# Kernel optimization log

Measured on AMD Instinct MI355X. Metric: run time of the kernel, lower is better.

## Reference

```python
import jax, jax.numpy as jnp
import numpy as np

S, N, NSUB, F, HID, NH = 8, 20000, 4000, 128, 64, 8


def setup_inputs() -> dict:
    key = jax.random.key(0)
    ks = jax.random.split(key, 24)
    # unique sorted node indices per snapshot (matches snap.nodes used for gather + scatter-pad)
    nodes = jnp.stack([jnp.sort(jax.random.permutation(ks[i], N)[:NSUB]) for i in range(S)])
    # dense normalized adjacency proxy (norm_adj.to_dense()); scaled so rows sum ~1
    adj = jax.random.uniform(ks[8], (S, NSUB, NSUB), dtype=jnp.float32) * (2.0 / NSUB)
    p = lambda k, shp: jax.random.normal(k, shp, dtype=jnp.float32) * 0.02
    return {
        "nodes": nodes,
        "adj": adj,
        "emb": p(ks[9], (N, F)),
        "W1": p(ks[10], (F, HID)), "b1": jnp.zeros((HID,), jnp.float32),
        "W2": p(ks[11], (HID, HID)), "b2": jnp.zeros((HID,), jnp.float32),
        "time_emb": p(ks[12], (2 * S - 1, NH)),
        "Wq": p(ks[13], (HID, HID)), "bq": jnp.zeros((HID,), jnp.float32),
        "Wk": p(ks[14], (HID, HID)), "bk": jnp.zeros((HID,), jnp.float32),
        "Wv": p(ks[15], (HID, HID)), "bv": jnp.zeros((HID,), jnp.float32),
        "Wo": p(ks[16], (HID, HID)), "bo": jnp.zeros((HID,), jnp.float32),
    }


def reference(nodes, adj, emb, W1, b1, W2, b2, time_emb,
              Wq, bq, Wk, bk, Wv, bv, Wo, bo):
    s, nsub = nodes.shape
    n_total, _ = emb.shape
    hid = W1.shape[1]
    nh = time_emb.shape[1]
    dh = hid // nh
    # per-snapshot GCN encode (2 layers of A @ (X W) + b, ReLU), vectorized over snapshots
    feat = emb[nodes]                                            # [S, n, F]
    h = jax.nn.relu(jnp.einsum('sij,sjh->sih', adj, feat @ W1) + b1)
    h = jax.nn.relu(jnp.einsum('sij,sjh->sih', adj, h @ W2) + b2)
    # scatter-pad into zero buffer of size nodes_num (output[pos_idx] = x)
    x = jnp.zeros((s, n_total, hid), h.dtype).at[jnp.arange(s)[:, None], nodes].set(h)
    x = x.transpose(1, 0, 2)                                     # [N, S, HID]
    # relative-position time bias: Embedding(2S-1, NH)[rel_matrix] -> [NH, S, S]
    rel = jnp.arange(s)[None, :] - jnp.arange(s)[:, None] + s - 1
    bias = time_emb[rel].transpose(2, 0, 1)
    # multi-head attention over the snapshot axis, batch = nodes
    q = (x @ Wq + bq).reshape(n_total, s, nh, dh) * (dh ** -0.5)
    k = (x @ Wk + bk).reshape(n_total, s, nh, dh)
    v = (x @ Wv + bv).reshape(n_total, s, nh, dh)
    scores = jnp.einsum('nqhd,nkhd->nhqk', q, k) + bias          # [N, NH, S, S]
    attn = jax.nn.softmax(scores, axis=-1)
    o = jnp.einsum('nhqk,nkhd->nqhd', attn, v).reshape(n_total, s, hid)
    o = o @ Wo + bo
    o = o.transpose(1, 0, 2)                                     # [S, N, HID]
    # gather active nodes back, then structure decoder z @ z.T per snapshot
    z = jnp.take_along_axis(o, nodes[:, :, None], axis=1)        # [S, n, HID]
    out = jnp.einsum('sid,sjd->sij', z, z)                       # [S, n, n]
    return out
```

## Files before the change

kernel.cpp:

```cpp
#include <hip/hip_runtime.h>
#include <hip/hip_bf16.h>
#include <cstdint>

#define S 8
#define NTOT 20000
#define NSUB 4000
#define NSUBP 4032
#define NST 63
#define F 128
#define HID 64
#define NH 8
#define DH 8

typedef __attribute__((ext_vector_type(8))) short bf16x8;
typedef __attribute__((ext_vector_type(4))) short bf16x4;
typedef __attribute__((ext_vector_type(4))) float f32x4;

__device__ __forceinline__ short f2bf(float f) {
  union { __hip_bfloat16 h; short s; } u;
  u.h = __float2bfloat16(f);
  return u.s;
}

__device__ __forceinline__ void gload16(const void* gsrc, void* ldst) {
  __builtin_amdgcn_global_load_lds(
      (const __attribute__((address_space(1))) void*)gsrc,
      (__attribute__((address_space(3))) void*)ldst, 16, 0, 0);
}

__global__ void k_pos_init(int* __restrict__ posIdx) {
  int t = blockIdx.x * 256 + threadIdx.x;
  if (t < NTOT * S) posIdx[t] = -1;
}

__global__ void k_pos_scatter(const int* __restrict__ nodes, int* __restrict__ posIdx) {
  int t = blockIdx.x * 256 + threadIdx.x;
  if (t < S * NSUB) {
    int s = t / NSUB, i = t - s * NSUB;
    posIdx[nodes[t] * S + s] = i;
  }
}

__global__ void k_pt_pad(short* __restrict__ Pt) {
  int t = blockIdx.x * 256 + threadIdx.x;
  int seg = t >> 2, off = (t & 3) * 8;
  bf16x8 z = (bf16x8){0,0,0,0,0,0,0,0};
  *(bf16x8*)(Pt + (size_t)seg * NSUBP + NSUB + off) = z;
}

__global__ __launch_bounds__(256) void k_feat_w1(const int* __restrict__ nodes,
                                                 const float* __restrict__ emb,
                                                 const float* __restrict__ W1,
                                                 short* __restrict__ Pt) {
  __shared__ __align__(16) float feat[16][F];
  __shared__ float tr[64][17];
  int t = threadIdx.x;
  int s = blockIdx.x / 250;
  int i0 = (blockIdx.x - s * 250) * 16;
  int gr0 = blockIdx.x * 16;
  int lr = t >> 4, lc = (t & 15) * 8;
  int n = nodes[gr0 + lr];
  *(f32x4*)&feat[lr][lc]     = *(const f32x4*)(emb + (size_t)n * F + lc);
  *(f32x4*)&feat[lr][lc + 4] = *(const f32x4*)(emb + (size_t)n * F + lc + 4);
  __syncthreads();
  int j = t & 63, ig = t >> 6;
  float acc[4] = {0.f, 0.f, 0.f, 0.f};
  for (int k = 0; k < F; ++k) {
    float w = W1[k * HID + j];
    #pragma unroll
    for (int i = 0; i < 4; ++i) acc[i] += feat[ig * 4 + i][k] * w;
  }
  #pragma unroll
  for (int i = 0; i < 4; ++i) tr[j][ig * 4 + i] = acc[i];
  __syncthreads();
  int jr = t >> 2, seg = (t & 3) * 4;
  bf16x4 o;
  #pragma unroll
  for (int u = 0; u < 4; ++u) o[u] = f2bf(tr[jr][seg + u]);
  *(bf16x4*)(Pt + ((size_t)s * HID + jr) * NSUBP + i0 + seg) = o;
}

template<int MODE>
__global__ __launch_bounds__(256) void k_adj(const float* __restrict__ adj,
                                             const short* __restrict__ Pt,
                                             const float* __restrict__ bias,
                                             float* __restrict__ out) {
  __shared__ __align__(16) float As[2][64 * 64];
  __shared__ __align__(16) short Bs[2][64 * 64];
  int bid = blockIdx.x;
  int s = bid & 7;
  int mb = bid >> 3;
  int tid = threadIdx.x;
  int w = tid >> 6, lane = tid & 63, l15 = lane & 15, g = lane >> 4;
  int m0 = mb * 64;
  const float* adjS = adj + (size_t)s * NSUB * NSUB;
  const short* PtS  = Pt  + (size_t)s * HID * NSUBP;

  int rbase = w * 4 + (lane >> 4);
  int sigA = l15;
  int clogA = (sigA & 8) | ((sigA & 7) ^ (rbase & 7));
  int acolf = clogA * 4;
  const float* arow[4];
  #pragma unroll
  for (int p = 0; p < 4; ++p) {
    int rg = m0 + p * 16 + rbase;
    rg = rg < NSUB ? rg : NSUB - 1;
    arow[p] = adjS + (size_t)rg * NSUB;
  }
  int sigB = lane & 7;
  int clogB = sigB ^ ((lane >> 3) & 7);
  const short* bsrc[2];
  #pragma unroll
  for (int p = 0; p < 2; ++p) {
    int col = p * 32 + w * 8 + (lane >> 3);
    bsrc[p] = PtS + (size_t)col * NSUBP + clogB * 8;
  }

  char* As0 = (char*)&As[0][0];
  char* Bs0 = (char*)&Bs[0][0];
  int wb = w * 1024;

  int arowf = w * 16 + l15;
  int aoff = arowf * 256 + (((2 * g) ^ (arowf & 7)) * 16);
  int boff[4];
  #pragma unroll
  for (int nf = 0; nf < 4; ++nf) {
    int col = nf * 16 + l15;
    boff[nf] = col * 128 + ((g ^ (col & 7)) * 16);
  }

  f32x4 acc[4];
  #pragma unroll
  for (int nf = 0; nf < 4; ++nf) acc[nf] = (f32x4){0.f, 0.f, 0.f, 0.f};

  #pragma unroll
  for (int p = 0; p < 4; ++p)
    gload16(arow[p] + acolf, As0 + p * 4096 + wb);
  #pragma unroll
  for (int p = 0; p < 2; ++p)
    gload16(bsrc[p], Bs0 + p * 4096 + wb);

  for (int t = 0; t < NST; ++t) {
    __syncthreads();
    int cur = t & 1;
    if (t + 1 < NST) {
      int kn = (t + 1) * 64;
      bool ok = (kn + acolf) < NSUB;
      const char* nA = As0 + (cur ^ 1) * 16384;
      const char* nB = Bs0 + (cur ^ 1) * 8192;
      #pragma unroll
      for (int p = 0; p < 4; ++p)
        gload16(ok ? (arow[p] + kn + acolf) : arow[p], (void*)(nA + p * 4096 + wb));
      #pragma unroll
      for (int p = 0; p < 2; ++p)
        gload16(bsrc[p] + kn, (void*)(nB + p * 4096 + wb));
    }
    const char* Ab = As0 + cur * 16384;
    const char* Bb = Bs0 + cur * 8192;
    f32x4 a0 = *(const f32x4*)(Ab + aoff);
    f32x4 a1 = *(const f32x4*)(Ab + (aoff ^ 16));
    f32x4 a2 = *(const f32x4*)(Ab + 128 + aoff);
    f32x4 a3 = *(const f32x4*)(Ab + 128 + (aoff ^ 16));
    bf16x8 af0, af1;
    af0[0] = f2bf(a0.x); af0[1] = f2bf(a0.y); af0[2] = f2bf(a0.z); af0[3] = f2bf(a0.w);
    af0[4] = f2bf(a1.x); af0[5] = f2bf(a1.y); af0[6] = f2bf(a1.z); af0[7] = f2bf(a1.w);
    af1[0] = f2bf(a2.x); af1[1] = f2bf(a2.y); af1[2] = f2bf(a2.z); af1[3] = f2bf(a2.w);
    af1[4] = f2bf(a3.x); af1[5] = f2bf(a3.y); af1[6] = f2bf(a3.z); af1[7] = f2bf(a3.w);
    #pragma unroll
    for (int nf = 0; nf < 4; ++nf) {
      bf16x8 b0 = *(const bf16x8*)(Bb + boff[nf]);
      bf16x8 b1 = *(const bf16x8*)(Bb + (boff[nf] ^ 64));
      acc[nf] = __builtin_amdgcn_mfma_f32_16x16x32_bf16(af0, b0, acc[nf], 0, 0, 0);
      acc[nf] = __builtin_amdgcn_mfma_f32_16x16x32_bf16(af1, b1, acc[nf], 0, 0, 0);
    }
  }

  float* P = out + (size_t)s * NSUB * HID;
  #pragma unroll
  for (int nf = 0; nf < 4; ++nf) {
    int col = nf * 16 + l15;
    float bv = (MODE == 1) ? bias[col] : 0.f;
    #pragma unroll
    for (int r = 0; r < 4; ++r) {
      int row = m0 + w * 16 + g * 4 + r;
      if (row < NSUB) {
        if (MODE == 1) P[(size_t)row * HID + col] = fmaxf(acc[nf][r] + bv, 0.f);
        else           P[(size_t)row * HID + col] = acc[nf][r];
      }
    }
  }
}

__global__ __launch_bounds__(256) void k_reduce1(const float* __restrict__ part,
                                                 const float* __restrict__ b1,
                                                 const float* __restrict__ W2,
                                                 short* __restrict__ Pt2) {
  __shared__ float h[32][65];
  int bid = blockIdx.x;
  int s = bid / 125, i0 = (bid - s * 125) * 32;
  int t = threadIdx.x;
  int r = t >> 3, c8 = (t & 7) * 8;
  const float* P0 = part + ((size_t)s * NSUB + i0 + r) * HID + c8;
  #pragma unroll
  for (int u = 0; u < 8; ++u)
    h[r][c8 + u] = fmaxf(P0[u] + b1[c8 + u], 0.f);
  __syncthreads();
  int j = t & 63, ib = t >> 6;
  float acc[8];
  #pragma unroll
  for (int u = 0; u < 8; ++u) acc[u] = 0.f;
  for (int k = 0; k < HID; ++k) {
    float w = W2[k * HID + j];
    #pragma unroll
    for (int u = 0; u < 8; ++u) acc[u] += h[ib * 8 + u][k] * w;
  }
  bf16x8 o;
  #pragma unroll
  for (int u = 0; u < 8; ++u) o[u] = f2bf(acc[u]);
  *(bf16x8*)(Pt2 + ((size_t)s * HID + j) * NSUBP + i0 + ib * 8) = o;
}

__global__ __launch_bounds__(256) void k_attn(const float* __restrict__ H,
                                              const int* __restrict__ posIdx,
                                              const float* __restrict__ Wq, const float* __restrict__ bq,
                                              const float* __restrict__ Wk, const float* __restrict__ bk,
                                              const float* __restrict__ Wv, const float* __restrict__ bv,
                                              const float* __restrict__ Wo, const float* __restrict__ bo,
                                              const float* __restrict__ te,
                                              short* __restrict__ Zb) {
  __shared__ __align__(16) float xk[4][S][HID];
  __shared__ __align__(16) float qs[4][S][HID];
  __shared__ __align__(16) float ks[4][S][HID];
  __shared__ __align__(16) float vs[4][S][HID];
  __shared__ __align__(16) float os[4][S][HID];
  int w = threadIdx.x >> 6;
  int lane = threadIdx.x & 63;
  int n = blockIdx.x * 4 + w;
  int pi[S];
  #pragma unroll
  for (int s = 0; s < S; ++s) {
    pi[s] = posIdx[n * S + s];
    xk[w][s][lane] = (pi[s] >= 0) ? H[((size_t)s * NSUB + pi[s]) * HID + lane] : 0.f;
  }
  __syncthreads();
  float aq[S], ak[S], av[S];
  #pragma unroll
  for (int s = 0; s < S; ++s) { aq[s] = bq[lane]; ak[s] = bk[lane]; av[s] = bv[lane]; }
  for (int k = 0; k < HID; ++k) {
    float wq = Wq[k*HID + lane], wk_ = Wk[k*HID + lane], wv = Wv[k*HID + lane];
    #pragma unroll
    for (int s = 0; s < S; ++s) {
      float xv = xk[w][s][k];
      aq[s] += xv * wq; ak[s] += xv * wk_; av[s] += xv * wv;
    }
  }
  const float qscale = 0.35355339059327373f;
  #pragma unroll
  for (int s = 0; s < S; ++s) {
    qs[w][s][lane] = aq[s] * qscale;
    ks[w][s][lane] = ak[s];
    vs[w][s][lane] = av[s];
  }
  __syncthreads();
  int h = lane >> 3, sq = lane & 7;
  f32x4 q0 = *(const f32x4*)&qs[w][sq][h * DH];
  f32x4 q1 = *(const f32x4*)&qs[w][sq][h * DH + 4];
  float sc[S];
  #pragma unroll
  for (int t = 0; t < S; ++t) {
    f32x4 k0v = *(const f32x4*)&ks[w][t][h * DH];
    f32x4 k1v = *(const f32x4*)&ks[w][t][h * DH + 4];
    float d = q0.x*k0v.x + q0.y*k0v.y + q0.z*k0v.z + q0.w*k0v.w
            + q1.x*k1v.x + q1.y*k1v.y + q1.z*k1v.z + q1.w*k1v.w;
    sc[t] = d + te[(t - sq + S - 1) * NH + h];
  }
  float m = sc[0];
  #pragma unroll
  for (int t = 1; t < S; ++t) m = fmaxf(m, sc[t]);
  float sum = 0.f;
  #pragma unroll
  for (int t = 0; t < S; ++t) { sc[t] = expf(sc[t] - m); sum += sc[t]; }
  float inv = 1.f / sum;
  f32x4 o0 = (f32x4){0.f,0.f,0.f,0.f}, o1 = (f32x4){0.f,0.f,0.f,0.f};
  #pragma unroll
  for (int t = 0; t < S; ++t) {
    f32x4 v0 = *(const f32x4*)&vs[w][t][h * DH];
    f32x4 v1 = *(const f32x4*)&vs[w][t][h * DH + 4];
    #pragma unroll
    for (int u = 0; u < 4; ++u) { o0[u] += sc[t] * v0[u]; o1[u] += sc[t] * v1[u]; }
  }
  #pragma unroll
  for (int u = 0; u < 4; ++u) { o0[u] *= inv; o1[u] *= inv; }
  *(f32x4*)&os[w][sq][h * DH]     = o0;
  *(f32x4*)&os[w][sq][h * DH + 4] = o1;
  __syncthreads();
  float ao[S];
  #pragma unroll
  for (int s = 0; s < S; ++s) ao[s] = bo[lane];
  for (int k = 0; k < HID; ++k) {
    float wo = Wo[k*HID + lane];
    #pragma unroll
    for (int s = 0; s < S; ++s) ao[s] += os[w][s][k] * wo;
  }
  #pragma unroll
  for (int s = 0; s < S; ++s)
    if (pi[s] >= 0) Zb[((size_t)s * NSUB + pi[s]) * HID + lane] = f2bf(ao[s]);
}

__global__ __launch_bounds__(256) void k_dec(const short* __restrict__ Zb,
                                             float* __restrict__ out) {
  __shared__ __align__(16) float tr[4][16][68];
  int bid = blockIdx.x;
  int s = bid & 7;
  int tt = bid >> 3;
  int by = tt / 63, bx = tt - by * 63;
  int wave = threadIdx.x >> 6, lane = threadIdx.x & 63;
  int l15 = lane & 15, g = lane >> 4;
  int m0 = by * 64 + wave * 16;
  int n0 = bx * 64;
  const short* ZS = Zb + (size_t)s * NSUB * HID;
  int mrow = m0 + l15;
  int mc = mrow < NSUB ? mrow : NSUB - 1;
  bf16x8 a0 = *(const bf16x8*)(ZS + (size_t)mc * HID + g * 8);
  bf16x8 a1 = *(const bf16x8*)(ZS + (size_t)mc * HID + 32 + g * 8);
  f32x4 acc[4];
  #pragma unroll
  for (int nf = 0; nf < 4; ++nf) acc[nf] = (f32x4){0.f, 0.f, 0.f, 0.f};
  #pragma unroll
  for (int nf = 0; nf < 4; ++nf) {
    int ncol = n0 + nf * 16 + l15;
    int nc = ncol < NSUB ? ncol : NSUB - 1;
    bf16x8 b0 = *(const bf16x8*)(ZS + (size_t)nc * HID + g * 8);
    bf16x8 b1 = *(const bf16x8*)(ZS + (size_t)nc * HID + 32 + g * 8);
    acc[nf] = __builtin_amdgcn_mfma_f32_16x16x32_bf16(a0, b0, acc[nf], 0, 0, 0);
    acc[nf] = __builtin_amdgcn_mfma_f32_16x16x32_bf16(a1, b1, acc[nf], 0, 0, 0);
  }
  #pragma unroll
  for (int nf = 0; nf < 4; ++nf)
    #pragma unroll
    for (int r = 0; r < 4; ++r)
      tr[wave][g * 4 + r][nf * 16 + l15] = acc[nf][r];
  __syncthreads();
  float* outS = out + (size_t)s * NSUB * NSUB;
  #pragma unroll
  for (int p = 0; p < 4; ++p) {
    int rr = p * 4 + g;
    int grow = m0 + rr;
    int gcol = n0 + l15 * 4;
    f32x4 v = *(const f32x4*)&tr[wave][rr][l15 * 4];
    if (grow < NSUB && gcol < NSUB)
      __builtin_nontemporal_store(v, (f32x4*)(outS + (size_t)grow * NSUB + gcol));
  }
}

extern "C" void kernel_launch(void* const* d_in, const int* in_sizes, int n_in,
                              void* d_out, int out_size, void* d_ws, size_t ws_size,
                              hipStream_t stream) {
  const int*   nodes = (const int*)d_in[0];
  const float* adj   = (const float*)d_in[1];
  const float* emb   = (const float*)d_in[2];
  const float* W1    = (const float*)d_in[3];
  const float* b1    = (const float*)d_in[4];
  const float* W2    = (const float*)d_in[5];
  const float* b2    = (const float*)d_in[6];
  const float* te    = (const float*)d_in[7];
  const float* Wq    = (const float*)d_in[8];
  const float* bq    = (const float*)d_in[9];
  const float* Wk    = (const float*)d_in[10];
  const float* bk    = (const float*)d_in[11];
  const float* Wv    = (const float*)d_in[12];
  const float* bv    = (const float*)d_in[13];
  const float* Wo    = (const float*)d_in[14];
  const float* bo    = (const float*)d_in[15];
  float* outp = (float*)d_out;

  float* part = (float*)d_ws;
  float* H    = part + (size_t)S * NSUB * HID;
  short* Pt   = (short*)(H + (size_t)S * NSUB * HID);
  short* Zb   = Pt + (size_t)S * HID * NSUBP;
  int* posIdx = (int*)(Zb + (size_t)S * NSUB * HID);

  k_pos_init<<<(NTOT*S + 255)/256, 256, 0, stream>>>(posIdx);
  k_pos_scatter<<<(S*NSUB + 255)/256, 256, 0, stream>>>(nodes, posIdx);
  k_pt_pad<<<8, 256, 0, stream>>>(Pt);

  k_feat_w1<<<2000, 256, 0, stream>>>(nodes, emb, W1, Pt);
  k_adj<0><<<504, 256, 0, stream>>>(adj, Pt, b1, part);
  k_reduce1<<<1000, 256, 0, stream>>>(part, b1, W2, Pt);
  k_adj<1><<<504, 256, 0, stream>>>(adj, Pt, b2, H);
  k_attn<<<NTOT/4, 256, 0, stream>>>(H, posIdx, Wq, bq, Wk, bk, Wv, bv, Wo, bo, te, Zb);
  k_dec<<<63*63*8, 256, 0, stream>>>(Zb, outp);
}
```

Before: 485.4 us.

## Retile adjacency GEMM to 16-row blocks with 128-wide K steps

The adjacency-times-features kernel moves from 64-row tiles over 504 blocks to 16-row tiles over 2000 blocks. Each wave now owns a 16-column slice of the 64 outputs, and the K step grows from 64 to 128 with matching XOR swizzles. The padded stride of the transposed feature buffer rises to 4096, and the pad kernel is resized to fill it. The aim is better occupancy and more bandwidth on the memory-bound read of adj; the cost is that each B tile is reused over fewer rows, so the bf16 feature matrix is read from L2 about four times as often.

New measurement: 559.9 us. 1.15x slower.

```diff
diff --git a/kernel.cpp b/kernel.cpp
--- a/kernel.cpp
+++ b/kernel.cpp
@@ -5,8 +5,7 @@
 #define S 8
 #define NTOT 20000
 #define NSUB 4000
-#define NSUBP 4032
-#define NST 63
+#define NSUBP 4096
 #define F 128
 #define HID 64
 #define NH 8
@@ -43,9 +42,9 @@
 
 __global__ void k_pt_pad(short* __restrict__ Pt) {
   int t = blockIdx.x * 256 + threadIdx.x;
-  int seg = t >> 2, off = (t & 3) * 8;
+  int row = t / 12, off = (t - row * 12) * 8;
   bf16x8 z = (bf16x8){0,0,0,0,0,0,0,0};
-  *(bf16x8*)(Pt + (size_t)seg * NSUBP + NSUB + off) = z;
+  *(bf16x8*)(Pt + (size_t)row * NSUBP + NSUB + off) = z;
 }
 
 __global__ __launch_bounds__(256) void k_feat_w1(const int* __restrict__ nodes,
@@ -85,109 +84,94 @@
                                              const short* __restrict__ Pt,
                                              const float* __restrict__ bias,
                                              float* __restrict__ out) {
-  __shared__ __align__(16) float As[2][64 * 64];
-  __shared__ __align__(16) short Bs[2][64 * 64];
+  __shared__ __align__(16) float As[2][16 * 128];
+  __shared__ __align__(16) short Bs[2][64 * 128];
   int bid = blockIdx.x;
-  int s = bid & 7;
-  int mb = bid >> 3;
+  int s = bid & 7, mb = bid >> 3;
+  int m0 = mb * 16;
   int tid = threadIdx.x;
   int w = tid >> 6, lane = tid & 63, l15 = lane & 15, g = lane >> 4;
-  int m0 = mb * 64;
   const float* adjS = adj + (size_t)s * NSUB * NSUB;
-  const short* PtS  = Pt  + (size_t)s * HID * NSUBP;
-
-  int rbase = w * 4 + (lane >> 4);
-  int sigA = l15;
-  int clogA = (sigA & 8) | ((sigA & 7) ^ (rbase & 7));
-  int acolf = clogA * 4;
-  const float* arow[4];
-  #pragma unroll
-  for (int p = 0; p < 4; ++p) {
-    int rg = m0 + p * 16 + rbase;
-    rg = rg < NSUB ? rg : NSUB - 1;
-    arow[p] = adjS + (size_t)rg * NSUB;
-  }
-  int sigB = lane & 7;
-  int clogB = sigB ^ ((lane >> 3) & 7);
-  const short* bsrc[2];
-  #pragma unroll
-  for (int p = 0; p < 2; ++p) {
-    int col = p * 32 + w * 8 + (lane >> 3);
-    bsrc[p] = PtS + (size_t)col * NSUBP + clogB * 8;
-  }
-
-  char* As0 = (char*)&As[0][0];
-  char* Bs0 = (char*)&Bs[0][0];
-  int wb = w * 1024;
-
-  int arowf = w * 16 + l15;
-  int aoff = arowf * 256 + (((2 * g) ^ (arowf & 7)) * 16);
-  int boff[4];
-  #pragma unroll
-  for (int nf = 0; nf < 4; ++nf) {
-    int col = nf * 16 + l15;
-    boff[nf] = col * 128 + ((g ^ (col & 7)) * 16);
-  }
-
-  f32x4 acc[4];
-  #pragma unroll
-  for (int nf = 0; nf < 4; ++nf) acc[nf] = (f32x4){0.f, 0.f, 0.f, 0.f};
-
-  #pragma unroll
-  for (int p = 0; p < 4; ++p)
-    gload16(arow[p] + acolf, As0 + p * 4096 + wb);
-  #pragma unroll
-  for (int p = 0; p < 2; ++p)
-    gload16(bsrc[p], Bs0 + p * 4096 + wb);
-
-  for (int t = 0; t < NST; ++t) {
+  const short* PtS  = Pt  + (size_t)s * HID * (size_t)NSUBP;
+
+  const float* asrc[2];
+  int aok[2], adst[2];
+  #pragma unroll
+  for (int q = 0; q < 2; ++q) {
+    int r = w * 4 + q * 2 + (lane >> 5);
+    int c = (lane & 31) ^ (r & 7);
+    asrc[q] = adjS + (size_t)(m0 + r) * NSUB + c * 4;
+    aok[q] = c * 4;
+    adst[q] = (w * 2 + q) * 1024;
+  }
+  const short* bsrc[4];
+  int bdst[4];
+  #pragma unroll
+  for (int q = 0; q < 4; ++q) {
+    int col = w * 16 + q * 4 + (lane >> 4);
+    int d = (lane & 15) ^ (col & 7);
+    bsrc[q] = PtS + (size_t)col * NSUBP + d * 8;
+    bdst[q] = (w * 4 + q) * 1024;
+  }
+
+  char* A0 = (char*)&As[0][0];
+  char* B0 = (char*)&Bs[0][0];
+
+  int aoff[4], boff[4];
+  int cl = w * 16 + l15;
+  #pragma unroll
+  for (int kk = 0; kk < 4; ++kk) {
+    int c0 = kk * 8 + g * 2;
+    aoff[kk] = l15 * 512 + ((c0 ^ (l15 & 7)) * 16);
+    boff[kk] = cl * 256 + (((kk * 4 + g) ^ (cl & 7)) * 16);
+  }
+
+  f32x4 acc = (f32x4){0.f, 0.f, 0.f, 0.f};
+
+  #pragma unroll
+  for (int q = 0; q < 2; ++q) gload16(asrc[q], A0 + adst[q]);
+  #pragma unroll
+  for (int q = 0; q < 4; ++q) gload16(bsrc[q], B0 + bdst[q]);
+
+  const int NSTEP = NSUBP / 128;
+  for (int t = 0; t < NSTEP; ++t) {
     __syncthreads();
     int cur = t & 1;
-    if (t + 1 < NST) {
-      int kn = (t + 1) * 64;
-      bool ok = (kn + acolf) < NSUB;
-      const char* nA = As0 + (cur ^ 1) * 16384;
-      const char* nB = Bs0 + (cur ^ 1) * 8192;
+    if (t + 1 < NSTEP) {
+      int kn = (t + 1) * 128;
+      char* nA = A0 + (cur ^ 1) * 8192;
+      char* nB = B0 + (cur ^ 1) * 16384;
       #pragma unroll
-      for (int p = 0; p < 4; ++p)
-        gload16(ok ? (arow[p] + kn + acolf) : arow[p], (void*)(nA + p * 4096 + wb));
+      for (int q = 0; q < 2; ++q) {
+        const float* sA = (kn + aok[q] < NSUB) ? (asrc[q] + kn) : asrc[q];
+        gload16(sA, nA + adst[q]);
+      }
       #pragma unroll
-      for (int p = 0; p < 2; ++p)
-        gload16(bsrc[p] + kn, (void*)(nB + p * 4096 + wb));
+      for (int q = 0; q < 4; ++q)
+        gload16(bsrc[q] + kn, nB + bdst[q]);
     }
-    const char* Ab = As0 + cur * 16384;
-    const char* Bb = Bs0 + cur * 8192;
-    f32x4 a0 = *(const f32x4*)(Ab + aoff);
-    f32x4 a1 = *(const f32x4*)(Ab + (aoff ^ 16));
-    f32x4 a2 = *(const f32x4*)(Ab + 128 + aoff);
-    f32x4 a3 = *(const f32x4*)(Ab + 128 + (aoff ^ 16));
-    bf16x8 af0, af1;
-    af0[0] = f2bf(a0.x); af0[1] = f2bf(a0.y); af0[2] = f2bf(a0.z); af0[3] = f2bf(a0.w);
-    af0[4] = f2bf(a1.x); af0[5] = f2bf(a1.y); af0[6] = f2bf(a1.z); af0[7] = f2bf(a1.w);
-    af1[0] = f2bf(a2.x); af1[1] = f2bf(a2.y); af1[2] = f2bf(a2.z); af1[3] = f2bf(a2.w);
-    af1[4] = f2bf(a3.x); af1[5] = f2bf(a3.y); af1[6] = f2bf(a3.z); af1[7] = f2bf(a3.w);
-    #pragma unroll
-    for (int nf = 0; nf < 4; ++nf) {
-      bf16x8 b0 = *(const bf16x8*)(Bb + boff[nf]);
-      bf16x8 b1 = *(const bf16x8*)(Bb + (boff[nf] ^ 64));
-      acc[nf] = __builtin_amdgcn_mfma_f32_16x16x32_bf16(af0, b0, acc[nf], 0, 0, 0);
-      acc[nf] = __builtin_amdgcn_mfma_f32_16x16x32_bf16(af1, b1, acc[nf], 0, 0, 0);
+    const char* Ab = A0 + cur * 8192;
+    const char* Bb = B0 + cur * 16384;
+    #pragma unroll
+    for (int kk = 0; kk < 4; ++kk) {
+      f32x4 a0 = *(const f32x4*)(Ab + aoff[kk]);
+      f32x4 a1 = *(const f32x4*)(Ab + (aoff[kk] ^ 16));
+      bf16x8 afr;
+      afr[0] = f2bf(a0.x); afr[1] = f2bf(a0.y); afr[2] = f2bf(a0.z); afr[3] = f2bf(a0.w);
+      afr[4] = f2bf(a1.x); afr[5] = f2bf(a1.y); afr[6] = f2bf(a1.z); afr[7] = f2bf(a1.w);
+      bf16x8 bfr = *(const bf16x8*)(Bb + boff[kk]);
+      acc = __builtin_amdgcn_mfma_f32_16x16x32_bf16(afr, bfr, acc, 0, 0, 0);
     }
   }
 
   float* P = out + (size_t)s * NSUB * HID;
-  #pragma unroll
-  for (int nf = 0; nf < 4; ++nf) {
-    int col = nf * 16 + l15;
-    float bv = (MODE == 1) ? bias[col] : 0.f;
-    #pragma unroll
-    for (int r = 0; r < 4; ++r) {
-      int row = m0 + w * 16 + g * 4 + r;
-      if (row < NSUB) {
-        if (MODE == 1) P[(size_t)row * HID + col] = fmaxf(acc[nf][r] + bv, 0.f);
-        else           P[(size_t)row * HID + col] = acc[nf][r];
-      }
-    }
+  float bv = (MODE == 1) ? bias[cl] : 0.f;
+  #pragma unroll
+  for (int r = 0; r < 4; ++r) {
+    int row = m0 + g * 4 + r;
+    float v = acc[r];
+    if (MODE == 1) v = fmaxf(v + bv, 0.f);
+    P[(size_t)row * HID + cl] = v;
   }
 }
 
@@ -382,12 +366,12 @@
 
   k_pos_init<<<(NTOT*S + 255)/256, 256, 0, stream>>>(posIdx);
   k_pos_scatter<<<(S*NSUB + 255)/256, 256, 0, stream>>>(nodes, posIdx);
-  k_pt_pad<<<8, 256, 0, stream>>>(Pt);
+  k_pt_pad<<<24, 256, 0, stream>>>(Pt);
 
   k_feat_w1<<<2000, 256, 0, stream>>>(nodes, emb, W1, Pt);
-  k_adj<0><<<504, 256, 0, stream>>>(adj, Pt, b1, part);
+  k_adj<0><<<2000, 256, 0, stream>>>(adj, Pt, b1, part);
   k_reduce1<<<1000, 256, 0, stream>>>(part, b1, W2, Pt);
-  k_adj<1><<<504, 256, 0, stream>>>(adj, Pt, b2, H);
+  k_adj<1><<<2000, 256, 0, stream>>>(adj, Pt, b2, H);
   k_attn<<<NTOT/4, 256, 0, stream>>>(H, posIdx, Wq, bq, Wk, bk, Wv, bv, Wo, bo, te, Zb);
   k_dec<<<63*63*8, 256, 0, stream>>>(Zb, outp);
 }
```
